# Kernel tuning notes

Measured on AMD Instinct MI355X. Metric: run time of the kernel, lower is better.

## Reference

```python
import jax, jax.numpy as jnp
import numpy as np


def setup_inputs() -> dict:
    key = jax.random.key(0)
    k1, k2, k3, k4 = jax.random.split(key, 4)
    B, C_in, C_out, E, K = 4, 128, 256, 30000, 5
    x = jax.random.normal(k1, (B, C_in, E, 1), dtype=jnp.float32)
    ne_idx = jax.random.randint(k2, (B, E, K - 1), 0, E, dtype=jnp.int32)
    conv_w = jax.random.normal(k3, (C_out, C_in, 1, K), dtype=jnp.float32) * 0.05
    conv_b = jax.random.normal(k4, (C_out,), dtype=jnp.float32) * 0.05
    return {"x": x, "ne_idx": ne_idx, "conv_w": conv_w, "conv_b": conv_b}


def reference(x, ne_idx, conv_w, conv_b):
    # x: [B, C, E, 1] edge features; ne_idx: [B, E, 4] neighbor edge ids.
    B, C, E, _ = x.shape
    xs = x[..., 0]                                        # [B, C, E]

    # pad_graph_mat: prepend self index column -> [B, E, 5]
    self_idx = jnp.broadcast_to(
        jnp.arange(E, dtype=ne_idx.dtype)[None, :, None], (B, E, 1))
    idx = jnp.concatenate([self_idx, ne_idx], axis=2) + 1  # +1 for zero pad slot

    # zero-pad feature dim so index 0 maps to zeros (matches torch padding col)
    x_pad = jnp.pad(xs, ((0, 0), (0, 0), (1, 0)))          # [B, C, E+1]

    # gather: f[b, c, e, k] = x_pad[b, c, idx[b, e, k]]
    f = jax.vmap(lambda xp, i: xp[:, i])(x_pad, idx)       # [B, C, E, 5]

    e0, e1, e2, e3, e4 = (f[..., j] for j in range(5))
    p = e1 + e3
    q = e2 + e4
    p1 = jnp.abs(e1 - e3)
    q1 = jnp.abs(e2 - e4)
    G = jnp.stack([e0, p, q, p1, q1], axis=-1)             # [B, C, E, 5]

    # Conv2d with kernel (1, 5): contraction over in-channels and the 5 taps
    out = jnp.einsum('bcek,ocuk->boe', G, conv_w) + conv_b[None, :, None]
    return out[..., None]                                  # [B, C_out, E, 1]
```

## Files before the change

### kernel.cpp

```cpp
#include <hip/hip_runtime.h>
#include <hip/hip_bf16.h>
#include <stdint.h>

#define E_N   30000
#define C_IN  128
#define C_OUT 256
#define B_N   4
#define KTAP  5
#define BN    64

typedef short bf16x8 __attribute__((ext_vector_type(8)));
typedef float f32x4  __attribute__((ext_vector_type(4)));

static __device__ __forceinline__ unsigned short f2bf(float f) {
    union { float f; uint32_t u; } v; v.f = f;
    uint32_t r = (v.u + 0x7FFFu + ((v.u >> 16) & 1u)) >> 16;
    return (unsigned short)r;
}
static __device__ __forceinline__ float bf2f(uint32_t h) {
    union { uint32_t u; float f; } v; v.u = h << 16;
    return v.f;
}

__global__ void pack_w_kernel(const float* __restrict__ w,
                              unsigned short* __restrict__ wp) {
    int tid = blockIdx.x * blockDim.x + threadIdx.x;
    if (tid >= 20 * 16 * 64) return;
    int s    = tid >> 10;
    int mt   = (tid >> 6) & 15;
    int lane = tid & 63;
    int m    = mt * 16 + (lane & 15);
    int kb   = s * 32 + ((lane >> 4) & 3) * 8;
    uint32_t pv[4];
    for (int jj = 0; jj < 4; ++jj) {
        unsigned short lo, hi;
        {
            int kk = kb + 2 * jj;
            int t = kk >> 7, c = kk & 127;
            lo = f2bf(w[(m * C_IN + c) * KTAP + t]);
        }
        {
            int kk = kb + 2 * jj + 1;
            int t = kk >> 7, c = kk & 127;
            hi = f2bf(w[(m * C_IN + c) * KTAP + t]);
        }
        pv[jj] = (uint32_t)lo | ((uint32_t)hi << 16);
    }
    uint4 val; val.x = pv[0]; val.y = pv[1]; val.z = pv[2]; val.w = pv[3];
    *(uint4*)(wp + (size_t)tid * 8) = val;
}

__global__ void transpose_kernel(const float* __restrict__ x,
                                 unsigned short* __restrict__ xT) {
    __shared__ float ld[C_IN][64 + 1];
    int b  = blockIdx.y;
    int e0 = blockIdx.x * 64;
    int t  = threadIdx.x;
    bool full = (e0 + 64 <= E_N);
    for (int pass = 0; pass < 8; ++pass) {
        int c  = pass * 16 + (t >> 4);
        int eo = (t & 15) * 4;
        if (full) {
            const float4 v = *(const float4*)(x + ((size_t)(b * C_IN + c) * E_N + e0 + eo));
            ld[c][eo] = v.x; ld[c][eo + 1] = v.y; ld[c][eo + 2] = v.z; ld[c][eo + 3] = v.w;
        } else {
            for (int i = 0; i < 4; ++i) {
                int e = e0 + eo + i;
                ld[c][eo + i] = (e < E_N) ? x[(size_t)(b * C_IN + c) * E_N + e] : 0.f;
            }
        }
    }
    __syncthreads();
    for (int pass = 0; pass < 4; ++pass) {
        int el = pass * 16 + (t >> 4);
        int c0 = (t & 15) * 8;
        int e  = e0 + el;
        if (e < E_N) {
            uint32_t pk[4];
            for (int i = 0; i < 4; ++i) {
                unsigned short lo = f2bf(ld[c0 + 2 * i][el]);
                unsigned short hi = f2bf(ld[c0 + 2 * i + 1][el]);
                pk[i] = (uint32_t)lo | ((uint32_t)hi << 16);
            }
            uint4 v; v.x = pk[0]; v.y = pk[1]; v.z = pk[2]; v.w = pk[3];
            *(uint4*)(xT + (size_t)(b * E_N + e) * C_IN + c0) = v;
        }
    }
}

__launch_bounds__(256)
__global__ void mesh_gemm(const unsigned short* __restrict__ wp,
                          const unsigned short* __restrict__ xT,
                          const int* __restrict__ ne,
                          const float* __restrict__ bias,
                          float* __restrict__ out) {
    __shared__ __align__(16) unsigned short gbuf[KTAP][BN][40];
    __shared__ int nbr[BN][4];

    const int b    = blockIdx.y;
    const int e0   = blockIdx.x * BN;
    const int tid  = threadIdx.x;
    const int lane = tid & 63;
    const int wave = tid >> 6;

    {
        int col = tid >> 2, j = tid & 3;
        int e = e0 + col; if (e >= E_N) e = E_N - 1;
        nbr[col][j] = ne[((size_t)b * E_N + e) * 4 + j];
    }
    __syncthreads();

    const int col = tid >> 2;
    const int c8  = (tid & 3) * 8;
    int self_e = e0 + col; if (self_e >= E_N) self_e = E_N - 1;
    const int s1 = nbr[col][0], s2 = nbr[col][2];
    const int s3 = nbr[col][1], s4 = nbr[col][3];

    const unsigned short* xb = xT + (size_t)b * E_N * C_IN + c8;
    const uint4* p0 = (const uint4*)(xb + (size_t)self_e * C_IN);
    const uint4* p1 = (const uint4*)(xb + (size_t)s1 * C_IN);
    const uint4* p2 = (const uint4*)(xb + (size_t)s2 * C_IN);
    const uint4* p3 = (const uint4*)(xb + (size_t)s3 * C_IN);
    const uint4* p4 = (const uint4*)(xb + (size_t)s4 * C_IN);

    f32x4 acc[4][4];
#pragma unroll
    for (int mt = 0; mt < 4; ++mt)
#pragma unroll
        for (int nt = 0; nt < 4; ++nt)
            acc[mt][nt] = (f32x4){0.f, 0.f, 0.f, 0.f};

    const uint4* wp16 = (const uint4*)wp;
    const int nl = lane & 15;
    const int k8 = (lane >> 4) * 8;

    uint4 v0 = p0[0], v1 = p1[0], v2 = p2[0], v3 = p3[0], v4 = p4[0];

#pragma unroll
    for (int cbi = 0; cbi < 4; ++cbi) {
        uint4 g1, g2, g3, g4;
        {
            const uint32_t* a = (const uint32_t*)&v1;
            const uint32_t* c = (const uint32_t*)&v2;
            uint32_t* o1 = (uint32_t*)&g1;
            uint32_t* o3 = (uint32_t*)&g3;
#pragma unroll
            for (int i = 0; i < 4; ++i) {
                float x0 = bf2f(a[i] & 0xFFFFu), x1 = bf2f(a[i] >> 16);
                float y0 = bf2f(c[i] & 0xFFFFu), y1 = bf2f(c[i] >> 16);
                o1[i] = (uint32_t)f2bf(x0 + y0) | ((uint32_t)f2bf(x1 + y1) << 16);
                o3[i] = (uint32_t)f2bf(fabsf(x0 - y0)) | ((uint32_t)f2bf(fabsf(x1 - y1)) << 16);
            }
            const uint32_t* d = (const uint32_t*)&v3;
            const uint32_t* e = (const uint32_t*)&v4;
            uint32_t* o2 = (uint32_t*)&g2;
            uint32_t* o4 = (uint32_t*)&g4;
#pragma unroll
            for (int i = 0; i < 4; ++i) {
                float x0 = bf2f(d[i] & 0xFFFFu), x1 = bf2f(d[i] >> 16);
                float y0 = bf2f(e[i] & 0xFFFFu), y1 = bf2f(e[i] >> 16);
                o2[i] = (uint32_t)f2bf(x0 + y0) | ((uint32_t)f2bf(x1 + y1) << 16);
                o4[i] = (uint32_t)f2bf(fabsf(x0 - y0)) | ((uint32_t)f2bf(fabsf(x1 - y1)) << 16);
            }
        }
        uint4 g0 = v0;

        __syncthreads();
        *(uint4*)(&gbuf[0][col][c8]) = g0;
        *(uint4*)(&gbuf[1][col][c8]) = g1;
        *(uint4*)(&gbuf[2][col][c8]) = g2;
        *(uint4*)(&gbuf[3][col][c8]) = g3;
        *(uint4*)(&gbuf[4][col][c8]) = g4;
        __syncthreads();

        if (cbi < 3) {
            v0 = p0[4 * (cbi + 1)];
            v1 = p1[4 * (cbi + 1)];
            v2 = p2[4 * (cbi + 1)];
            v3 = p3[4 * (cbi + 1)];
            v4 = p4[4 * (cbi + 1)];
        }

#pragma unroll
        for (int t = 0; t < KTAP; ++t) {
            const int s = t * 4 + cbi;
            bf16x8 af[4];
#pragma unroll
            for (int mt = 0; mt < 4; ++mt) {
                uint4 w4 = wp16[(s * 16 + wave * 4 + mt) * 64 + lane];
                af[mt] = *(bf16x8*)&w4;
            }
#pragma unroll
            for (int nt = 0; nt < 4; ++nt) {
                bf16x8 bf = *(const bf16x8*)(&gbuf[t][nt * 16 + nl][k8]);
#pragma unroll
                for (int mt = 0; mt < 4; ++mt)
                    acc[mt][nt] = __builtin_amdgcn_mfma_f32_16x16x32_bf16(
                        af[mt], bf, acc[mt][nt], 0, 0, 0);
            }
        }
    }

    const int quad = lane >> 4;
    const int ecol = lane & 15;
#pragma unroll
    for (int mt = 0; mt < 4; ++mt) {
        int o_base = (wave * 4 + mt) * 16 + quad * 4;
#pragma unroll
        for (int r = 0; r < 4; ++r) {
            int o = o_base + r;
            float bv = bias[o];
#pragma unroll
            for (int nt = 0; nt < 4; ++nt) {
                int e = e0 + nt * 16 + ecol;
                if (e < E_N)
                    __builtin_nontemporal_store(
                        acc[mt][nt][r] + bv,
                        &out[((size_t)(b * C_OUT + o)) * E_N + e]);
            }
        }
    }
}

__global__ void fallback_kernel(const float* __restrict__ x,
                                const int* __restrict__ ne,
                                const float* __restrict__ w,
                                const float* __restrict__ bias,
                                float* __restrict__ out) {
    size_t id = (size_t)blockIdx.x * blockDim.x + threadIdx.x;
    if (id >= (size_t)B_N * C_OUT * E_N) return;
    int e = (int)(id % E_N);
    int o = (int)((id / E_N) % C_OUT);
    int b = (int)(id / ((size_t)E_N * C_OUT));
    const int4 nb = *(const int4*)(ne + ((size_t)b * E_N + e) * 4);
    float acc = bias[o];
    for (int c = 0; c < C_IN; ++c) {
        const float* xb = x + (size_t)(b * C_IN + c) * E_N;
        float s0 = xb[e];
        float x1 = xb[nb.x], x2 = xb[nb.y], x3 = xb[nb.z], x4 = xb[nb.w];
        const float* wo = w + (size_t)(o * C_IN + c) * KTAP;
        acc += wo[0] * s0
             + wo[1] * (x1 + x3)
             + wo[2] * (x2 + x4)
             + wo[3] * fabsf(x1 - x3)
             + wo[4] * fabsf(x2 - x4);
    }
    out[id] = acc;
}

extern "C" void kernel_launch(void* const* d_in, const int* in_sizes, int n_in,
                              void* d_out, int out_size, void* d_ws, size_t ws_size,
                              hipStream_t stream) {
    const float* x      = (const float*)d_in[0];
    const int*   ne_idx = (const int*)d_in[1];
    const float* conv_w = (const float*)d_in[2];
    const float* conv_b = (const float*)d_in[3];
    float* out = (float*)d_out;

    const size_t xT_off = 512 * 1024;
    const size_t need   = xT_off + (size_t)B_N * E_N * C_IN * 2;

    if (ws_size < need) {
        size_t total = (size_t)B_N * C_OUT * E_N;
        int blocks = (int)((total + 255) / 256);
        fallback_kernel<<<blocks, 256, 0, stream>>>(x, ne_idx, conv_w, conv_b, out);
        return;
    }

    unsigned short* wp = (unsigned short*)d_ws;
    unsigned short* xT = (unsigned short*)((char*)d_ws + xT_off);

    pack_w_kernel<<<80, 256, 0, stream>>>(conv_w, wp);
    dim3 tg((E_N + 63) / 64, B_N);
    transpose_kernel<<<tg, 256, 0, stream>>>(x, xT);
    dim3 gg((E_N + BN - 1) / BN, B_N);
    mesh_gemm<<<gg, 256, 0, stream>>>(wp, xT, ne_idx, conv_b, out);
}
```

Measured before the change: 262.0 us.

## Stage full gathered tile in swizzled LDS once, use 512 threads per block

Result: faster. 238.5 us (-9.0%).

```diff
diff --git a/kernel.cpp b/kernel.cpp
--- a/kernel.cpp
+++ b/kernel.cpp
@@ -20,6 +20,21 @@
 static __device__ __forceinline__ float bf2f(uint32_t h) {
     union { uint32_t u; float f; } v; v.u = h << 16;
     return v.f;
+}
+
+static __device__ __forceinline__ void comb8(const uint4& u, const uint4& v,
+                                             uint4& s, uint4& d) {
+    const uint32_t* a = (const uint32_t*)&u;
+    const uint32_t* b = (const uint32_t*)&v;
+    uint32_t* so = (uint32_t*)&s;
+    uint32_t* dr = (uint32_t*)&d;
+#pragma unroll
+    for (int i = 0; i < 4; ++i) {
+        float x0 = bf2f(a[i] & 0xFFFFu), x1 = bf2f(a[i] >> 16);
+        float y0 = bf2f(b[i] & 0xFFFFu), y1 = bf2f(b[i] >> 16);
+        so[i] = (uint32_t)f2bf(x0 + y0) | ((uint32_t)f2bf(x1 + y1) << 16);
+        dr[i] = (uint32_t)f2bf(fabsf(x0 - y0)) | ((uint32_t)f2bf(fabsf(x1 - y1)) << 16);
+    }
 }
 
 __global__ void pack_w_kernel(const float* __restrict__ w,
@@ -88,14 +103,13 @@
     }
 }
 
-__launch_bounds__(256)
+__launch_bounds__(512, 4)
 __global__ void mesh_gemm(const unsigned short* __restrict__ wp,
                           const unsigned short* __restrict__ xT,
                           const int* __restrict__ ne,
                           const float* __restrict__ bias,
                           float* __restrict__ out) {
-    __shared__ __align__(16) unsigned short gbuf[KTAP][BN][40];
-    __shared__ int nbr[BN][4];
+    __shared__ uint4 gbuf[KTAP][BN][16];
 
     const int b    = blockIdx.y;
     const int e0   = blockIdx.x * BN;
@@ -104,119 +118,76 @@
     const int wave = tid >> 6;
 
     {
-        int col = tid >> 2, j = tid & 3;
+        const int col = tid >> 3;
+        const int ci  = tid & 7;
         int e = e0 + col; if (e >= E_N) e = E_N - 1;
-        nbr[col][j] = ne[((size_t)b * E_N + e) * 4 + j];
+        const int4 nb = *(const int4*)(ne + ((size_t)b * E_N + e) * 4);
+
+        const unsigned short* xb = xT + (size_t)b * E_N * C_IN;
+        const uint4* r0 = (const uint4*)(xb + (size_t)e    * C_IN) + ci;
+        const uint4* r1 = (const uint4*)(xb + (size_t)nb.x * C_IN) + ci;
+        const uint4* r2 = (const uint4*)(xb + (size_t)nb.y * C_IN) + ci;
+        const uint4* r3 = (const uint4*)(xb + (size_t)nb.z * C_IN) + ci;
+        const uint4* r4 = (const uint4*)(xb + (size_t)nb.w * C_IN) + ci;
+
+        uint4 a0 = r0[0], a1 = r1[0], a2 = r2[0], a3 = r3[0], a4 = r4[0];
+        uint4 b0 = r0[8], b1 = r1[8], b2 = r2[8], b3 = r3[8], b4 = r4[8];
+
+        const int sw = col & 15;
+        const int cl = ci ^ sw;
+        const int ch = (ci + 8) ^ sw;
+
+        uint4 s, d;
+        gbuf[0][col][cl] = a0;
+        comb8(a1, a3, s, d);  gbuf[1][col][cl] = s;  gbuf[3][col][cl] = d;
+        comb8(a2, a4, s, d);  gbuf[2][col][cl] = s;  gbuf[4][col][cl] = d;
+        gbuf[0][col][ch] = b0;
+        comb8(b1, b3, s, d);  gbuf[1][col][ch] = s;  gbuf[3][col][ch] = d;
+        comb8(b2, b4, s, d);  gbuf[2][col][ch] = s;  gbuf[4][col][ch] = d;
     }
     __syncthreads();
 
-    const int col = tid >> 2;
-    const int c8  = (tid & 3) * 8;
-    int self_e = e0 + col; if (self_e >= E_N) self_e = E_N - 1;
-    const int s1 = nbr[col][0], s2 = nbr[col][2];
-    const int s3 = nbr[col][1], s4 = nbr[col][3];
-
-    const unsigned short* xb = xT + (size_t)b * E_N * C_IN + c8;
-    const uint4* p0 = (const uint4*)(xb + (size_t)self_e * C_IN);
-    const uint4* p1 = (const uint4*)(xb + (size_t)s1 * C_IN);
-    const uint4* p2 = (const uint4*)(xb + (size_t)s2 * C_IN);
-    const uint4* p3 = (const uint4*)(xb + (size_t)s3 * C_IN);
-    const uint4* p4 = (const uint4*)(xb + (size_t)s4 * C_IN);
-
-    f32x4 acc[4][4];
-#pragma unroll
-    for (int mt = 0; mt < 4; ++mt)
+    f32x4 acc[2][4];
+#pragma unroll
+    for (int mt = 0; mt < 2; ++mt)
 #pragma unroll
         for (int nt = 0; nt < 4; ++nt)
             acc[mt][nt] = (f32x4){0.f, 0.f, 0.f, 0.f};
 
     const uint4* wp16 = (const uint4*)wp;
     const int nl = lane & 15;
-    const int k8 = (lane >> 4) * 8;
-
-    uint4 v0 = p0[0], v1 = p1[0], v2 = p2[0], v3 = p3[0], v4 = p4[0];
-
-#pragma unroll
-    for (int cbi = 0; cbi < 4; ++cbi) {
-        uint4 g1, g2, g3, g4;
-        {
-            const uint32_t* a = (const uint32_t*)&v1;
-            const uint32_t* c = (const uint32_t*)&v2;
-            uint32_t* o1 = (uint32_t*)&g1;
-            uint32_t* o3 = (uint32_t*)&g3;
-#pragma unroll
-            for (int i = 0; i < 4; ++i) {
-                float x0 = bf2f(a[i] & 0xFFFFu), x1 = bf2f(a[i] >> 16);
-                float y0 = bf2f(c[i] & 0xFFFFu), y1 = bf2f(c[i] >> 16);
-                o1[i] = (uint32_t)f2bf(x0 + y0) | ((uint32_t)f2bf(x1 + y1) << 16);
-                o3[i] = (uint32_t)f2bf(fabsf(x0 - y0)) | ((uint32_t)f2bf(fabsf(x1 - y1)) << 16);
-            }
-            const uint32_t* d = (const uint32_t*)&v3;
-            const uint32_t* e = (const uint32_t*)&v4;
-            uint32_t* o2 = (uint32_t*)&g2;
-            uint32_t* o4 = (uint32_t*)&g4;
-#pragma unroll
-            for (int i = 0; i < 4; ++i) {
-                float x0 = bf2f(d[i] & 0xFFFFu), x1 = bf2f(d[i] >> 16);
-                float y0 = bf2f(e[i] & 0xFFFFu), y1 = bf2f(e[i] >> 16);
-                o2[i] = (uint32_t)f2bf(x0 + y0) | ((uint32_t)f2bf(x1 + y1) << 16);
-                o4[i] = (uint32_t)f2bf(fabsf(x0 - y0)) | ((uint32_t)f2bf(fabsf(x1 - y1)) << 16);
-            }
-        }
-        uint4 g0 = v0;
-
-        __syncthreads();
-        *(uint4*)(&gbuf[0][col][c8]) = g0;
-        *(uint4*)(&gbuf[1][col][c8]) = g1;
-        *(uint4*)(&gbuf[2][col][c8]) = g2;
-        *(uint4*)(&gbuf[3][col][c8]) = g3;
-        *(uint4*)(&gbuf[4][col][c8]) = g4;
-        __syncthreads();
-
-        if (cbi < 3) {
-            v0 = p0[4 * (cbi + 1)];
-            v1 = p1[4 * (cbi + 1)];
-            v2 = p2[4 * (cbi + 1)];
-            v3 = p3[4 * (cbi + 1)];
-            v4 = p4[4 * (cbi + 1)];
-        }
-
-#pragma unroll
-        for (int t = 0; t < KTAP; ++t) {
-            const int s = t * 4 + cbi;
-            bf16x8 af[4];
-#pragma unroll
-            for (int mt = 0; mt < 4; ++mt) {
-                uint4 w4 = wp16[(s * 16 + wave * 4 + mt) * 64 + lane];
-                af[mt] = *(bf16x8*)&w4;
-            }
-#pragma unroll
-            for (int nt = 0; nt < 4; ++nt) {
-                bf16x8 bf = *(const bf16x8*)(&gbuf[t][nt * 16 + nl][k8]);
-#pragma unroll
-                for (int mt = 0; mt < 4; ++mt)
-                    acc[mt][nt] = __builtin_amdgcn_mfma_f32_16x16x32_bf16(
-                        af[mt], bf, acc[mt][nt], 0, 0, 0);
-            }
+    const int kq = lane >> 4;
+
+#pragma unroll 4
+    for (int s = 0; s < 20; ++s) {
+        const int tap = s >> 2, cbi = s & 3;
+        uint4 w0 = wp16[(s * 16 + wave * 2 + 0) * 64 + lane];
+        uint4 w1 = wp16[(s * 16 + wave * 2 + 1) * 64 + lane];
+        bf16x8 af0 = *(bf16x8*)&w0;
+        bf16x8 af1 = *(bf16x8*)&w1;
+#pragma unroll
+        for (int nt = 0; nt < 4; ++nt) {
+            uint4 bv = gbuf[tap][nt * 16 + nl][((cbi << 2) + kq) ^ nl];
+            bf16x8 bf = *(bf16x8*)&bv;
+            acc[0][nt] = __builtin_amdgcn_mfma_f32_16x16x32_bf16(af0, bf, acc[0][nt], 0, 0, 0);
+            acc[1][nt] = __builtin_amdgcn_mfma_f32_16x16x32_bf16(af1, bf, acc[1][nt], 0, 0, 0);
         }
     }
 
     const int quad = lane >> 4;
     const int ecol = lane & 15;
 #pragma unroll
-    for (int mt = 0; mt < 4; ++mt) {
-        int o_base = (wave * 4 + mt) * 16 + quad * 4;
+    for (int mt = 0; mt < 2; ++mt) {
+        int ob = (wave * 2 + mt) * 16 + quad * 4;
 #pragma unroll
         for (int r = 0; r < 4; ++r) {
-            int o = o_base + r;
+            int o = ob + r;
             float bv = bias[o];
 #pragma unroll
             for (int nt = 0; nt < 4; ++nt) {
                 int e = e0 + nt * 16 + ecol;
                 if (e < E_N)
-                    __builtin_nontemporal_store(
-                        acc[mt][nt][r] + bv,
-                        &out[((size_t)(b * C_OUT + o)) * E_N + e]);
+                    out[((size_t)(b * C_OUT + o)) * E_N + e] = acc[mt][nt][r] + bv;
             }
         }
     }
@@ -274,5 +245,5 @@
     dim3 tg((E_N + 63) / 64, B_N);
     transpose_kernel<<<tg, 256, 0, stream>>>(x, xT);
     dim3 gg((E_N + BN - 1) / BN, B_N);
-    mesh_gemm<<<gg, 256, 0, stream>>>(wp, xT, ne_idx, conv_b, out);
-}
+    mesh_gemm<<<gg, 512, 0, stream>>>(wp, xT, ne_idx, conv_b, out);
+}
```
